# Optimization experiments

Measured on AMD Instinct MI355X. Metric: run time of the kernel, lower is better.

## Reference

```python
import jax, jax.numpy as jnp
import numpy as np
from jax import lax

B, T, D = 16, 2048, 1024
MASK_VAL = -1e30  # float32 path in the torch module


def setup_inputs() -> dict:
    key = jax.random.key(0)
    ks = jax.random.split(key, 10)
    s = 1.0 / np.sqrt(D)
    return {
        "query": jax.random.normal(ks[0], (B, T, D), jnp.float32),
        "value": jax.random.normal(ks[1], (B, T, D), jnp.float32),
        "mask": jnp.zeros((B, T), jnp.bool_),
        "last_attn": jax.random.uniform(ks[2], (B, T), jnp.float32),
        "conv_w": jax.random.normal(ks[3], (D, 1, 3), jnp.float32) * 0.3,   # OIH
        "conv_b": jax.random.normal(ks[4], (D,), jnp.float32) * 0.02,
        "Wq": jax.random.normal(ks[5], (D, D), jnp.float32) * s,
        "Wv": jax.random.normal(ks[6], (D, D), jnp.float32) * s,
        "w_score": jax.random.normal(ks[7], (D,), jnp.float32) * s,
        "b_score": jax.random.normal(ks[8], (), jnp.float32) * 0.02,
        "bias": jax.random.uniform(ks[9], (D,), jnp.float32, -0.1, 0.1),
    }


def reference(query, value, mask, last_attn, conv_w, conv_b, Wq, Wv, w_score, b_score, bias):
    # conv1d(1 -> D, k=3, pad=1) over last_attn: (B,1,T) -> (B,D,T) -> (B,T,D)
    conv = lax.conv_general_dilated(
        last_attn[:, None, :], conv_w, window_strides=(1,), padding=[(1, 1)],
        dimension_numbers=("NCH", "OIH", "NCH"))
    conv_attn = jnp.transpose(conv + conv_b[None, :, None], (0, 2, 1))  # (B,T,D)

    q = jnp.einsum("btd,ed->bte", query, Wq)   # query_proj (no bias)
    v = jnp.einsum("btd,ed->bte", value, Wv)   # value_proj (no bias)
    energy = jnp.tanh(q + v + conv_attn + bias)            # (B,T,D)
    score = jnp.einsum("btd,d->bt", energy, w_score) + b_score  # (B,T)

    score = jnp.where(mask, MASK_VAL, score)
    # smoothing=True branch: sigmoid then L1 normalize
    sc = jax.nn.sigmoid(score)
    attn = sc / jnp.sum(sc, axis=-1, keepdims=True)        # (B,T)

    context = jnp.einsum("bt,btd->bd", attn, value)        # (B,D)
    return context, attn
```

## Files before the change

kernel.cpp:

```cpp
#include <hip/hip_runtime.h>
#include <math.h>


typedef _Float16 f16;
typedef _Float16 f16x4 __attribute__((ext_vector_type(4)));
typedef _Float16 f16x8 __attribute__((ext_vector_type(8)));
typedef __fp16   h16x2 __attribute__((ext_vector_type(2)));
typedef float f32x4 __attribute__((ext_vector_type(4)));

__global__ void k_convert_w(const float* __restrict__ Wq, const float* __restrict__ Wv,
                            f16* __restrict__ Wc) {
    int idx = (blockIdx.x * 256 + threadIdx.x) * 4;
    int e = idx >> 11;
    int k = idx & 2047;
    const float* src = (k < 1024) ? (Wq + e * 1024 + k) : (Wv + e * 1024 + (k - 1024));
    float4 w = *(const float4*)src;
    f16x4 o = { (f16)w.x, (f16)w.y, (f16)w.z, (f16)w.w };
    *(f16x4*)(Wc + idx) = o;
}

__global__ void __launch_bounds__(256) k_gemm_score(
    const float* __restrict__ query, const float* __restrict__ value,
    const f16* __restrict__ Wc,
    const float* __restrict__ last_attn,
    const float* __restrict__ conv_w, const float* __restrict__ conv_b,
    const float* __restrict__ w_score, const float* __restrict__ bias,
    float* __restrict__ score)
{
    __shared__ __align__(16) char smem[16384 + 8192];
    char* As = smem;
    char* Bs = smem + 16384;

    const int tid  = threadIdx.x;
    const int lane = tid & 63;
    const int wid  = tid >> 6;
    const int wm   = wid >> 1, wn = wid & 1;

    int bid = blockIdx.x;
    int x = bid & 7, s = bid >> 3;
    int m_tile = (x << 5) + (s >> 3);
    int n_tile = s & 7;
    long m0 = (long)m_tile << 7;
    int  n0 = n_tile << 7;

    long aoff[4]; char* adst[4];
#pragma unroll
    for (int i = 0; i < 4; ++i) {
        int idx = i * 256 + tid;
        int r  = idx >> 3;
        int cb = (idx & 7) << 4;
        int cbs = cb ^ ((r & 7) << 4);
        aoff[i] = (m0 + r) * 1024 + (cbs >> 2);
        adst[i] = As + idx * 16;
    }
    long boff[2]; char* bdst[2];
#pragma unroll
    for (int i = 0; i < 2; ++i) {
        int idx = i * 256 + tid;
        int r  = idx >> 2;
        int cb = (idx & 3) << 4;
        int cbs = cb ^ ((r & 3) << 4);
        boff[i] = (long)(n0 + r) * 2048 + (cbs >> 1);
        bdst[i] = Bs + idx * 16;
    }

    int aRd[4][2], bRd[4];
#pragma unroll
    for (int mi = 0; mi < 4; ++mi) {
        int row = wm * 64 + mi * 16 + (lane & 15);
        int cb0 = (lane >> 4) * 32;
        int sw  = (row & 7) << 4;
        aRd[mi][0] = row * 128 + (cb0 ^ sw);
        aRd[mi][1] = row * 128 + ((cb0 + 16) ^ sw);
    }
#pragma unroll
    for (int ni = 0; ni < 4; ++ni) {
        int e  = wn * 64 + ni * 16 + (lane & 15);
        int cb = (lane >> 4) * 16;
        bRd[ni] = e * 64 + (cb ^ ((e & 3) << 4));
    }

    f32x4 acc[4][4] = {};

#define K_STEP(src, k0x, k0g)                                                      \
    {                                                                              \
        __syncthreads();                                                           \
        _Pragma("unroll")                                                          \
        for (int i = 0; i < 4; ++i)                                                \
            __builtin_amdgcn_global_load_lds(                                      \
                (const __attribute__((address_space(1))) void*)(src + aoff[i] + (k0x)), \
                (__attribute__((address_space(3))) void*)(adst[i]), 16, 0, 0);     \
        _Pragma("unroll")                                                          \
        for (int i = 0; i < 2; ++i)                                                \
            __builtin_amdgcn_global_load_lds(                                      \
                (const __attribute__((address_space(1))) void*)(Wc + boff[i] + (k0g)), \
                (__attribute__((address_space(3))) void*)(bdst[i]), 16, 0, 0);     \
        __syncthreads();                                                           \
        f16x8 aF[4], bF[4];                                                        \
        _Pragma("unroll")                                                          \
        for (int mi = 0; mi < 4; ++mi) {                                           \
            float4 x0 = *(const float4*)(As + aRd[mi][0]);                         \
            float4 x1 = *(const float4*)(As + aRd[mi][1]);                         \
            union { f16x8 v; h16x2 h[4]; } u;                                      \
            u.h[0] = __builtin_amdgcn_cvt_pkrtz(x0.x, x0.y);                       \
            u.h[1] = __builtin_amdgcn_cvt_pkrtz(x0.z, x0.w);                       \
            u.h[2] = __builtin_amdgcn_cvt_pkrtz(x1.x, x1.y);                       \
            u.h[3] = __builtin_amdgcn_cvt_pkrtz(x1.z, x1.w);                       \
            aF[mi] = u.v;                                                          \
        }                                                                          \
        _Pragma("unroll")                                                          \
        for (int ni = 0; ni < 4; ++ni)                                             \
            bF[ni] = *(const f16x8*)(Bs + bRd[ni]);                                \
        _Pragma("unroll")                                                          \
        for (int mi = 0; mi < 4; ++mi)                                             \
            _Pragma("unroll")                                                      \
            for (int ni = 0; ni < 4; ++ni)                                         \
                acc[mi][ni] = __builtin_amdgcn_mfma_f32_16x16x32_f16(              \
                    aF[mi], bF[ni], acc[mi][ni], 0, 0, 0);                         \
    }

    for (int kt = 0; kt < 32; ++kt)  K_STEP(query, kt * 32, kt * 32);
    for (int kt = 0; kt < 32; ++kt)  K_STEP(value, kt * 32, 1024 + kt * 32);
#undef K_STEP

    float wsc[4], c0[4], c1[4], c2[4], cbb[4];
#pragma unroll
    for (int ni = 0; ni < 4; ++ni) {
        int c = n0 + wn * 64 + ni * 16 + (lane & 15);
        wsc[ni] = w_score[c];
        c0[ni] = conv_w[3 * c];
        c1[ni] = conv_w[3 * c + 1];
        c2[ni] = conv_w[3 * c + 2];
        cbb[ni] = conv_b[c] + bias[c];
    }
    int bb = (int)(m0 >> 11);
    int t0 = (int)(m0 & 2047);
    const float* la = last_attn + bb * 2048;
    float* sc = score + bb * 2048;
#pragma unroll
    for (int mi = 0; mi < 4; ++mi) {
#pragma unroll
        for (int r = 0; r < 4; ++r) {
            int tl = t0 + wm * 64 + mi * 16 + ((lane >> 4) << 2) + r;
            float lm = (tl > 0)    ? la[tl - 1] : 0.f;
            float l0 = la[tl];
            float lp = (tl < 2047) ? la[tl + 1] : 0.f;
            float sacc = 0.f;
#pragma unroll
            for (int ni = 0; ni < 4; ++ni) {
                float val = acc[mi][ni][r] + c0[ni] * lm + c1[ni] * l0 + c2[ni] * lp + cbb[ni];
                sacc += wsc[ni] * tanhf(val);
            }
            sacc += __shfl_xor(sacc, 1);
            sacc += __shfl_xor(sacc, 2);
            sacc += __shfl_xor(sacc, 4);
            sacc += __shfl_xor(sacc, 8);
            if ((lane & 15) == 0) atomicAdd(sc + tl, sacc);
        }
    }
}

__global__ void k_normalize(float* __restrict__ score, const unsigned char* __restrict__ mask,
                            const float* __restrict__ b_score)
{
    int b = blockIdx.x;
    int tid = threadIdx.x;
    float bs = b_score[0];
    float vals[8];
    float loc = 0.f;
#pragma unroll
    for (int j = 0; j < 8; ++j) {
        int t = j * 256 + tid;
        float xv = score[b * 2048 + t] + bs;
        if (mask[b * 2048 + t]) xv = -1e30f;
        float sg = 1.f / (1.f + expf(-xv));
        vals[j] = sg;
        loc += sg;
    }
#pragma unroll
    for (int off = 1; off < 64; off <<= 1) loc += __shfl_xor(loc, off);
    __shared__ float red[4];
    if ((tid & 63) == 0) red[tid >> 6] = loc;
    __syncthreads();
    float inv = 1.f / (red[0] + red[1] + red[2] + red[3]);
#pragma unroll
    for (int j = 0; j < 8; ++j) {
        int t = j * 256 + tid;
        score[b * 2048 + t] = vals[j] * inv;
    }
}

__global__ void k_context(const float* __restrict__ value, const float* __restrict__ attn,
                          float* __restrict__ ctx)
{
    int bidx = blockIdx.x;
    int b  = bidx >> 5;
    int tc = bidx & 31;
    int t0 = tc * 64;
    int tid = threadIdx.x;
    const float4* v4 = (const float4*)(value + (long)(b * 2048 + t0) * 1024) + tid;
    const float* at = attn + b * 2048 + t0;
    float4 a = { 0.f, 0.f, 0.f, 0.f };
    for (int t = 0; t < 64; ++t) {
        float w = at[t];
        float4 v = v4[t * 256];
        a.x += w * v.x; a.y += w * v.y; a.z += w * v.z; a.w += w * v.w;
    }
    float* o = ctx + b * 1024 + tid * 4;
    atomicAdd(o + 0, a.x);
    atomicAdd(o + 1, a.y);
    atomicAdd(o + 2, a.z);
    atomicAdd(o + 3, a.w);
}

extern "C" void kernel_launch(void* const* d_in, const int* in_sizes, int n_in,
                              void* d_out, int out_size, void* d_ws, size_t ws_size,
                              hipStream_t stream)
{
    const float*          query     = (const float*)d_in[0];
    const float*          value     = (const float*)d_in[1];
    const unsigned char*  mask      = (const unsigned char*)d_in[2];
    const float*          last_attn = (const float*)d_in[3];
    const float*          conv_w    = (const float*)d_in[4];
    const float*          conv_b    = (const float*)d_in[5];
    const float*          Wq        = (const float*)d_in[6];
    const float*          Wv        = (const float*)d_in[7];
    const float*          w_score   = (const float*)d_in[8];
    const float*          b_score   = (const float*)d_in[9];
    const float*          bias      = (const float*)d_in[10];

    f16* Wc = (f16*)d_ws;
    if (ws_size < (size_t)4 * 1024 * 1024) return;

    float* out  = (float*)d_out;
    float* ctx  = out;
    float* attn = out + 16 * 1024;

    (void)hipMemsetAsync(attn, 0, 16 * 2048 * 4, stream);
    (void)hipMemsetAsync(ctx, 0, 16 * 1024 * 4, stream);
    k_convert_w<<<2048, 256, 0, stream>>>(Wq, Wv, Wc);
    k_gemm_score<<<2048, 256, 0, stream>>>(query, value, Wc, last_attn,
                                           conv_w, conv_b, w_score, bias, attn);
    k_normalize<<<16, 256, 0, stream>>>(attn, mask, b_score);
    k_context<<<512, 256, 0, stream>>>(value, attn, ctx);
}
```

Before: 555.2 us.

## Pre-convert activations to fp16 and use async global-to-LDS loads in GEMM

Adds a conversion pass that writes query and value (concatenated along K) as fp16 into a 128MB workspace alongside the fp16 weights. A new GEMM kernel then streams the fp16 activations directly into LDS with global_load_lds and runs MFMA on them, keeping the fused conv/bias/tanh/score epilogue. The goal is to remove in-GEMM fp32-to-fp16 conversion and register staging, at the cost of an extra full pass over the activations (read fp32, write fp16). The old path is kept as a fallback when the workspace is too small.

```diff
diff --git a/kernel.cpp b/kernel.cpp
--- a/kernel.cpp
+++ b/kernel.cpp
@@ -7,6 +7,150 @@
 typedef _Float16 f16x8 __attribute__((ext_vector_type(8)));
 typedef __fp16   h16x2 __attribute__((ext_vector_type(2)));
 typedef float f32x4 __attribute__((ext_vector_type(4)));
+
+__global__ void k_convert(const float* __restrict__ query, const float* __restrict__ value,
+                          const float* __restrict__ Wq, const float* __restrict__ Wv,
+                          f16* __restrict__ Xc, f16* __restrict__ Wc)
+{
+    long g = (long)blockIdx.x * 256 + threadIdx.x;
+    if (blockIdx.x < 65536) {
+        long idx = g * 4;
+        long m = idx >> 11;
+        int  k = (int)(idx & 2047);
+        const float* src = (k < 1024) ? (query + m * 1024 + k)
+                                      : (value + m * 1024 + (k - 1024));
+        float4 w = *(const float4*)src;
+        f16x4 o = { (f16)w.x, (f16)w.y, (f16)w.z, (f16)w.w };
+        *(f16x4*)(Xc + idx) = o;
+    } else {
+        long idx = (g - (long)65536 * 256) * 4;
+        long e = idx >> 11;
+        int  k = (int)(idx & 2047);
+        const float* src = (k < 1024) ? (Wq + e * 1024 + k)
+                                      : (Wv + e * 1024 + (k - 1024));
+        float4 w = *(const float4*)src;
+        f16x4 o = { (f16)w.x, (f16)w.y, (f16)w.z, (f16)w.w };
+        *(f16x4*)(Wc + idx) = o;
+    }
+}
+
+__global__ void __launch_bounds__(256) k_gemm_f16(
+    const f16* __restrict__ Xc, const f16* __restrict__ Wc,
+    const float* __restrict__ last_attn,
+    const float* __restrict__ conv_w, const float* __restrict__ conv_b,
+    const float* __restrict__ w_score, const float* __restrict__ bias,
+    float* __restrict__ score)
+{
+    __shared__ __align__(16) char smem[8192 + 8192];
+    char* As = smem;
+    char* Bs = smem + 8192;
+
+    const int tid  = threadIdx.x;
+    const int lane = tid & 63;
+    const int wid  = tid >> 6;
+    const int wm   = wid >> 1, wn = wid & 1;
+
+    int bid = blockIdx.x;
+    int x = bid & 7, s = bid >> 3;
+    int m_tile = (x << 5) + (s >> 3);
+    int n_tile = s & 7;
+    long m0 = (long)m_tile << 7;
+    int  n0 = n_tile << 7;
+
+    long aoff[2]; char* adst[2];
+    long boff[2]; char* bdst[2];
+#pragma unroll
+    for (int i = 0; i < 2; ++i) {
+        int idx = i * 256 + tid;
+        int r  = idx >> 2;
+        int cb = (idx & 3) << 4;
+        int cbs = cb ^ ((r & 3) << 4);
+        aoff[i] = (m0 + r) * 2048 + (cbs >> 1);
+        adst[i] = As + idx * 16;
+        boff[i] = (long)(n0 + r) * 2048 + (cbs >> 1);
+        bdst[i] = Bs + idx * 16;
+    }
+
+    int aRd[4], bRd[4];
+#pragma unroll
+    for (int mi = 0; mi < 4; ++mi) {
+        int row = wm * 64 + mi * 16 + (lane & 15);
+        int cb  = (lane >> 4) * 16;
+        aRd[mi] = row * 64 + (cb ^ ((row & 3) << 4));
+    }
+#pragma unroll
+    for (int ni = 0; ni < 4; ++ni) {
+        int e  = wn * 64 + ni * 16 + (lane & 15);
+        int cb = (lane >> 4) * 16;
+        bRd[ni] = e * 64 + (cb ^ ((e & 3) << 4));
+    }
+
+    f32x4 acc[4][4] = {};
+
+    for (int kt = 0; kt < 64; ++kt) {
+        int k0 = kt * 32;
+        __syncthreads();
+#pragma unroll
+        for (int i = 0; i < 2; ++i)
+            __builtin_amdgcn_global_load_lds(
+                (const __attribute__((address_space(1))) void*)(Xc + aoff[i] + k0),
+                (__attribute__((address_space(3))) void*)(adst[i]), 16, 0, 0);
+#pragma unroll
+        for (int i = 0; i < 2; ++i)
+            __builtin_amdgcn_global_load_lds(
+                (const __attribute__((address_space(1))) void*)(Wc + boff[i] + k0),
+                (__attribute__((address_space(3))) void*)(bdst[i]), 16, 0, 0);
+        __syncthreads();
+
+        f16x8 aF[4], bF[4];
+#pragma unroll
+        for (int mi = 0; mi < 4; ++mi) aF[mi] = *(const f16x8*)(As + aRd[mi]);
+#pragma unroll
+        for (int ni = 0; ni < 4; ++ni) bF[ni] = *(const f16x8*)(Bs + bRd[ni]);
+#pragma unroll
+        for (int mi = 0; mi < 4; ++mi)
+#pragma unroll
+            for (int ni = 0; ni < 4; ++ni)
+                acc[mi][ni] = __builtin_amdgcn_mfma_f32_16x16x32_f16(
+                    aF[mi], bF[ni], acc[mi][ni], 0, 0, 0);
+    }
+
+    float wsc[4], c0[4], c1[4], c2[4], cbb[4];
+#pragma unroll
+    for (int ni = 0; ni < 4; ++ni) {
+        int c = n0 + wn * 64 + ni * 16 + (lane & 15);
+        wsc[ni] = w_score[c];
+        c0[ni] = conv_w[3 * c];
+        c1[ni] = conv_w[3 * c + 1];
+        c2[ni] = conv_w[3 * c + 2];
+        cbb[ni] = conv_b[c] + bias[c];
+    }
+    int bb = (int)(m0 >> 11);
+    int t0 = (int)(m0 & 2047);
+    const float* la = last_attn + bb * 2048;
+    float* sc = score + bb * 2048;
+#pragma unroll
+    for (int mi = 0; mi < 4; ++mi) {
+#pragma unroll
+        for (int r = 0; r < 4; ++r) {
+            int tl = t0 + wm * 64 + mi * 16 + ((lane >> 4) << 2) + r;
+            float lm = (tl > 0)    ? la[tl - 1] : 0.f;
+            float l0 = la[tl];
+            float lp = (tl < 2047) ? la[tl + 1] : 0.f;
+            float sacc = 0.f;
+#pragma unroll
+            for (int ni = 0; ni < 4; ++ni) {
+                float val = acc[mi][ni][r] + c0[ni] * lm + c1[ni] * l0 + c2[ni] * lp + cbb[ni];
+                sacc += wsc[ni] * tanhf(val);
+            }
+            sacc += __shfl_xor(sacc, 1);
+            sacc += __shfl_xor(sacc, 2);
+            sacc += __shfl_xor(sacc, 4);
+            sacc += __shfl_xor(sacc, 8);
+            if ((lane & 15) == 0) atomicAdd(sc + tl, sacc);
+        }
+    }
+}
 
 __global__ void k_convert_w(const float* __restrict__ Wq, const float* __restrict__ Wv,
                             f16* __restrict__ Wc) {
@@ -229,18 +373,31 @@
     const float*          b_score   = (const float*)d_in[9];
     const float*          bias      = (const float*)d_in[10];
 
-    f16* Wc = (f16*)d_ws;
-    if (ws_size < (size_t)4 * 1024 * 1024) return;
-
     float* out  = (float*)d_out;
     float* ctx  = out;
     float* attn = out + 16 * 1024;
 
     (void)hipMemsetAsync(attn, 0, 16 * 2048 * 4, stream);
     (void)hipMemsetAsync(ctx, 0, 16 * 1024 * 4, stream);
-    k_convert_w<<<2048, 256, 0, stream>>>(Wq, Wv, Wc);
-    k_gemm_score<<<2048, 256, 0, stream>>>(query, value, Wc, last_attn,
-                                           conv_w, conv_b, w_score, bias, attn);
+
+    const size_t xbytes = (size_t)32768 * 2048 * 2;
+    const size_t wbytes = (size_t)1024 * 2048 * 2;
+
+    if (ws_size >= xbytes + wbytes) {
+        f16* Xc = (f16*)d_ws;
+        f16* Wc = (f16*)((char*)d_ws + xbytes);
+        k_convert<<<65536 + 2048, 256, 0, stream>>>(query, value, Wq, Wv, Xc, Wc);
+        k_gemm_f16<<<2048, 256, 0, stream>>>(Xc, Wc, last_attn,
+                                             conv_w, conv_b, w_score, bias, attn);
+    } else if (ws_size >= wbytes) {
+        f16* Wc = (f16*)d_ws;
+        k_convert_w<<<2048, 256, 0, stream>>>(Wq, Wv, Wc);
+        k_gemm_score<<<2048, 256, 0, stream>>>(query, value, Wc, last_attn,
+                                               conv_w, conv_b, w_score, bias, attn);
+    } else {
+        return;
+    }
+
     k_normalize<<<16, 256, 0, stream>>>(attn, mask, b_score);
     k_context<<<512, 256, 0, stream>>>(value, attn, ctx);
 }
```

Measured after the change: 544.4 us. About the same (-1.9%).
